# Kernel tuning notes

Hardware: AMD Instinct MI355X
Metric: run time of the kernel (lower is better)

Reference implementation:

```python
import jax, jax.numpy as jnp
import numpy as np
import math

SUB = 0.8  # fraction of input capsules kept


def _capsule_weighted_average(u):
    # u: [B, I, O, D]
    n = jnp.linalg.norm(u, axis=3, keepdims=True)          # [B, I, O, 1]
    num = jnp.sum(u * n, axis=1)                           # [B, O, D]
    den = jnp.sum(n, axis=1)                               # [B, O, 1]
    return num / den


def setup_inputs() -> dict:
    key = jax.random.key(0)
    B, I, O, D = 128, 1152, 32, 16
    u_predict = jax.random.normal(key, (B, I, O, D), dtype=jnp.float32)
    return {"u_predict": u_predict}


def reference(u_predict) -> jnp.ndarray:
    B, I, O, D = u_predict.shape
    subset_size = math.ceil(SUB * I)  # kth smallest along input_caps dim

    v = _capsule_weighted_average(u_predict)               # [B, O, D]

    # metric == 'mse': losses = -<v, u_ij> over the capsule dim
    losses = -jnp.einsum('bod,biod->bio', v, u_predict)    # [B, I, O]

    # kthvalue(k=subset_size, dim=1): k-th smallest along axis 1
    loss_threshold = jnp.sort(losses, axis=1)[:, subset_size - 1, :]  # [B, O]

    choose = (losses <= loss_threshold[:, None, :]).astype(u_predict.dtype)  # [B, I, O]
    u_masked = u_predict * choose[..., None]               # [B, I, O, D]

    return _capsule_weighted_average(u_masked)             # [B, O, D]
```

## Files before the change

kernel.cpp:

```cpp
#include <hip/hip_runtime.h>
#include <math.h>

#define BLOCK   384
#define I_CAPS  1152
#define O_CAPS  32
#define D_DIM   16
#define ROWS    3
#define K_SEL   922
#define NWAVES  6

__device__ __forceinline__ float wave_reduce_sum(float v) {
    #pragma unroll
    for (int off = 32; off > 0; off >>= 1) v += __shfl_down(v, off);
    return v;
}

__global__ __launch_bounds__(BLOCK, 3)
void subset_routing_kernel(const float* __restrict__ u, float* __restrict__ out) {
    __shared__ float red[NWAVES][17];
    __shared__ float sh_v[D_DIM];
    __shared__ int   hist[256];
    __shared__ unsigned sh_prefix;
    __shared__ int   sh_k;

    const int t    = threadIdx.x;
    const int lane = t & 63;
    const int wave = t >> 6;

    int X = blockIdx.x;
    int r = X & 7;
    int m = (X >> 3) & 1;
    int q = X >> 4;
    int p = q * 8 + r;
    int b = p >> 4;
    int o = ((p & 15) << 1) | m;

    const float4* base =
        (const float4*)u + (((size_t)b * I_CAPS) * O_CAPS + (size_t)o) * (D_DIM / 4);

    float uu[ROWS][D_DIM];
    float nn[ROWS];
    #pragma unroll
    for (int rr = 0; rr < ROWS; ++rr) {
        int i = t + rr * BLOCK;
        const float4* rowp = base + (size_t)i * (O_CAPS * (D_DIM / 4));
        float4 a0 = rowp[0], a1 = rowp[1], a2 = rowp[2], a3 = rowp[3];
        uu[rr][ 0]=a0.x; uu[rr][ 1]=a0.y; uu[rr][ 2]=a0.z; uu[rr][ 3]=a0.w;
        uu[rr][ 4]=a1.x; uu[rr][ 5]=a1.y; uu[rr][ 6]=a1.z; uu[rr][ 7]=a1.w;
        uu[rr][ 8]=a2.x; uu[rr][ 9]=a2.y; uu[rr][10]=a2.z; uu[rr][11]=a2.w;
        uu[rr][12]=a3.x; uu[rr][13]=a3.y; uu[rr][14]=a3.z; uu[rr][15]=a3.w;
    }

    float num_acc[D_DIM];
    #pragma unroll
    for (int d = 0; d < D_DIM; ++d) num_acc[d] = 0.f;
    float den_acc = 0.f;
    #pragma unroll
    for (int rr = 0; rr < ROWS; ++rr) {
        float s = 0.f;
        #pragma unroll
        for (int d = 0; d < D_DIM; ++d) s += uu[rr][d] * uu[rr][d];
        nn[rr] = sqrtf(s);
        den_acc += nn[rr];
        #pragma unroll
        for (int d = 0; d < D_DIM; ++d) num_acc[d] += uu[rr][d] * nn[rr];
    }

    #pragma unroll
    for (int d = 0; d < D_DIM; ++d) {
        float s = wave_reduce_sum(num_acc[d]);
        if (lane == 0) red[wave][d] = s;
    }
    {
        float s = wave_reduce_sum(den_acc);
        if (lane == 0) red[wave][16] = s;
    }
    __syncthreads();
    if (t < D_DIM) {
        float tot = 0.f, dtot = 0.f;
        #pragma unroll
        for (int w = 0; w < NWAVES; ++w) { tot += red[w][t]; dtot += red[w][16]; }
        sh_v[t] = tot / dtot;
    }
    __syncthreads();

    float vv[D_DIM];
    #pragma unroll
    for (int d = 0; d < D_DIM; ++d) vv[d] = sh_v[d];

    unsigned key[ROWS];
    #pragma unroll
    for (int rr = 0; rr < ROWS; ++rr) {
        float loss = 0.f;
        #pragma unroll
        for (int d = 0; d < D_DIM; ++d) loss += vv[d] * uu[rr][d];
        loss = -loss;
        unsigned bits = __float_as_uint(loss);
        unsigned msk  = ((unsigned)((int)bits >> 31)) | 0x80000000u;
        key[rr] = bits ^ msk;
    }

    unsigned prefix = 0u;
    int kk = K_SEL;
    #pragma unroll
    for (int shift = 24; shift >= 0; shift -= 8) {
        if (t < 256) hist[t] = 0;
        __syncthreads();
        unsigned maskAbove = (shift == 24) ? 0u : (0xFFFFFFFFu << (shift + 8));
        #pragma unroll
        for (int rr = 0; rr < ROWS; ++rr) {
            unsigned k = key[rr];
            if ((k & maskAbove) == prefix)
                atomicAdd(&hist[(k >> shift) & 255u], 1);
        }
        __syncthreads();
        if (wave == 0) {
            int c0 = hist[lane*4+0], c1 = hist[lane*4+1],
                c2 = hist[lane*4+2], c3 = hist[lane*4+3];
            int s = c0 + c1 + c2 + c3;
            int cum = s;
            #pragma unroll
            for (int off = 1; off < 64; off <<= 1) {
                int vsh = __shfl_up(cum, off);
                if (lane >= off) cum += vsh;
            }
            int cumprev = cum - s;
            bool has = (cumprev < kk) && (cum >= kk);
            unsigned long long ball = __ballot(has);
            int win = __ffsll(ball) - 1;
            if (lane == win) {
                int kr = kk - cumprev;
                int digit = 0;
                if (kr > c0) { kr -= c0; digit = 1;
                    if (kr > c1) { kr -= c1; digit = 2;
                        if (kr > c2) { kr -= c2; digit = 3; } } }
                sh_prefix = prefix | ((unsigned)(lane*4 + digit) << shift);
                sh_k = kr;
            }
        }
        __syncthreads();
        prefix = sh_prefix;
        kk = sh_k;
    }

    float num2[D_DIM];
    #pragma unroll
    for (int d = 0; d < D_DIM; ++d) num2[d] = 0.f;
    float den2 = 0.f;
    #pragma unroll
    for (int rr = 0; rr < ROWS; ++rr) {
        float msk = (key[rr] <= prefix) ? 1.0f : 0.0f;
        float w = nn[rr] * msk;
        den2 += w;
        #pragma unroll
        for (int d = 0; d < D_DIM; ++d) num2[d] += uu[rr][d] * w;
    }

    #pragma unroll
    for (int d = 0; d < D_DIM; ++d) {
        float s = wave_reduce_sum(num2[d]);
        if (lane == 0) red[wave][d] = s;
    }
    {
        float s = wave_reduce_sum(den2);
        if (lane == 0) red[wave][16] = s;
    }
    __syncthreads();
    if (t < D_DIM) {
        float tot = 0.f, dtot = 0.f;
        #pragma unroll
        for (int w = 0; w < NWAVES; ++w) { tot += red[w][t]; dtot += red[w][16]; }
        out[(((size_t)b * O_CAPS) + o) * D_DIM + t] = tot / dtot;
    }
}

extern "C" void kernel_launch(void* const* d_in, const int* in_sizes, int n_in,
                              void* d_out, int out_size, void* d_ws, size_t ws_size,
                              hipStream_t stream) {
    const float* u = (const float*)d_in[0];
    float* out = (float*)d_out;
    const int B = 128;
    subset_routing_kernel<<<dim3(B * O_CAPS), dim3(BLOCK), 0, stream>>>(u, out);
}
```

Baseline: 452.0 us.

## Split each capsule row across four lanes with DPP reductions

Reassigns work so four adjacent lanes each load one float4 of a 16-float capsule row, giving fully coalesced 64-byte segments per row and 12 rows per thread group. Norms and dot products are completed with DPP cross-lane swaps, and the norm is recomputed in the second pass instead of being held in registers. Because each key now appears four times, the radix-select rank and the denominator are scaled by four. The aim is better load coalescing and lower register pressure (launch bounds raised to 5) for higher occupancy, at the cost of 4x more shared-memory histogram atomics.

```diff
diff --git a/kernel.cpp b/kernel.cpp
--- a/kernel.cpp
+++ b/kernel.cpp
@@ -5,19 +5,21 @@
 #define I_CAPS  1152
 #define O_CAPS  32
 #define D_DIM   16
-#define ROWS    3
-#define K_SEL   922
+#define RPT     12
+#define K_SEL4  3688
 #define NWAVES  6
 
-__device__ __forceinline__ float wave_reduce_sum(float v) {
-    #pragma unroll
-    for (int off = 32; off > 0; off >>= 1) v += __shfl_down(v, off);
-    return v;
+__device__ __forceinline__ float dpp_xor1(float x) {
+    return __int_as_float(__builtin_amdgcn_mov_dpp(__float_as_int(x), 0xB1, 0xF, 0xF, true));
+}
+__device__ __forceinline__ float dpp_xor2(float x) {
+    return __int_as_float(__builtin_amdgcn_mov_dpp(__float_as_int(x), 0x4E, 0xF, 0xF, true));
 }
 
-__global__ __launch_bounds__(BLOCK, 3)
+__global__ __launch_bounds__(BLOCK, 5)
 void subset_routing_kernel(const float* __restrict__ u, float* __restrict__ out) {
-    __shared__ float red[NWAVES][17];
+    __shared__ float sh_num[NWAVES][16];
+    __shared__ float sh_den[NWAVES];
     __shared__ float sh_v[D_DIM];
     __shared__ int   hist[256];
     __shared__ unsigned sh_prefix;
@@ -26,90 +28,72 @@
     const int t    = threadIdx.x;
     const int lane = t & 63;
     const int wave = t >> 6;
+    const int c    = t & 3;
+    const int s    = t >> 2;
 
     int X = blockIdx.x;
-    int r = X & 7;
-    int m = (X >> 3) & 1;
-    int q = X >> 4;
-    int p = q * 8 + r;
-    int b = p >> 4;
-    int o = ((p & 15) << 1) | m;
+    int r8 = X & 7, mm = (X >> 3) & 1, q8 = X >> 4;
+    int p  = q8 * 8 + r8;
+    int b  = p >> 4;
+    int o  = ((p & 15) << 1) | mm;
 
-    const float4* base =
-        (const float4*)u + (((size_t)b * I_CAPS) * O_CAPS + (size_t)o) * (D_DIM / 4);
+    const float* base = u + (((size_t)b * I_CAPS) * O_CAPS + (size_t)o) * D_DIM + c * 4;
 
-    float uu[ROWS][D_DIM];
-    float nn[ROWS];
+    float4 q[RPT];
     #pragma unroll
-    for (int rr = 0; rr < ROWS; ++rr) {
-        int i = t + rr * BLOCK;
-        const float4* rowp = base + (size_t)i * (O_CAPS * (D_DIM / 4));
-        float4 a0 = rowp[0], a1 = rowp[1], a2 = rowp[2], a3 = rowp[3];
-        uu[rr][ 0]=a0.x; uu[rr][ 1]=a0.y; uu[rr][ 2]=a0.z; uu[rr][ 3]=a0.w;
-        uu[rr][ 4]=a1.x; uu[rr][ 5]=a1.y; uu[rr][ 6]=a1.z; uu[rr][ 7]=a1.w;
-        uu[rr][ 8]=a2.x; uu[rr][ 9]=a2.y; uu[rr][10]=a2.z; uu[rr][11]=a2.w;
-        uu[rr][12]=a3.x; uu[rr][13]=a3.y; uu[rr][14]=a3.z; uu[rr][15]=a3.w;
+    for (int r = 0; r < RPT; ++r)
+        q[r] = *(const float4*)(base + (size_t)(r * 96 + s) * (O_CAPS * D_DIM));
+
+    float ax = 0.f, ay = 0.f, az = 0.f, aw = 0.f, dn = 0.f;
+    #pragma unroll
+    for (int r = 0; r < RPT; ++r) {
+        float ss = q[r].x*q[r].x + q[r].y*q[r].y + q[r].z*q[r].z + q[r].w*q[r].w;
+        ss += dpp_xor1(ss); ss += dpp_xor2(ss);
+        float n = sqrtf(ss);
+        ax += q[r].x * n; ay += q[r].y * n; az += q[r].z * n; aw += q[r].w * n;
+        dn += n;
     }
-
-    float num_acc[D_DIM];
     #pragma unroll
-    for (int d = 0; d < D_DIM; ++d) num_acc[d] = 0.f;
-    float den_acc = 0.f;
-    #pragma unroll
-    for (int rr = 0; rr < ROWS; ++rr) {
-        float s = 0.f;
+    for (int off = 4; off < 64; off <<= 1) {
+        ax += __shfl_down(ax, off); ay += __shfl_down(ay, off);
+        az += __shfl_down(az, off); aw += __shfl_down(aw, off);
+        dn += __shfl_down(dn, off);
+    }
+    dn += dpp_xor1(dn); dn += dpp_xor2(dn);
+    if (lane < 4) {
+        float* dst = &sh_num[wave][lane * 4];
+        dst[0] = ax; dst[1] = ay; dst[2] = az; dst[3] = aw;
+    }
+    if (lane == 0) sh_den[wave] = dn;
+    __syncthreads();
+    if (t < D_DIM) {
+        float nm = 0.f, dd = 0.f;
         #pragma unroll
-        for (int d = 0; d < D_DIM; ++d) s += uu[rr][d] * uu[rr][d];
-        nn[rr] = sqrtf(s);
-        den_acc += nn[rr];
-        #pragma unroll
-        for (int d = 0; d < D_DIM; ++d) num_acc[d] += uu[rr][d] * nn[rr];
-    }
-
-    #pragma unroll
-    for (int d = 0; d < D_DIM; ++d) {
-        float s = wave_reduce_sum(num_acc[d]);
-        if (lane == 0) red[wave][d] = s;
-    }
-    {
-        float s = wave_reduce_sum(den_acc);
-        if (lane == 0) red[wave][16] = s;
+        for (int w = 0; w < NWAVES; ++w) { nm += sh_num[w][t]; dd += sh_den[w]; }
+        sh_v[t] = nm / (dd * 0.25f);
     }
     __syncthreads();
-    if (t < D_DIM) {
-        float tot = 0.f, dtot = 0.f;
-        #pragma unroll
-        for (int w = 0; w < NWAVES; ++w) { tot += red[w][t]; dtot += red[w][16]; }
-        sh_v[t] = tot / dtot;
-    }
-    __syncthreads();
+    float4 v4 = make_float4(sh_v[c*4+0], sh_v[c*4+1], sh_v[c*4+2], sh_v[c*4+3]);
 
-    float vv[D_DIM];
+    unsigned key[RPT];
     #pragma unroll
-    for (int d = 0; d < D_DIM; ++d) vv[d] = sh_v[d];
-
-    unsigned key[ROWS];
-    #pragma unroll
-    for (int rr = 0; rr < ROWS; ++rr) {
-        float loss = 0.f;
-        #pragma unroll
-        for (int d = 0; d < D_DIM; ++d) loss += vv[d] * uu[rr][d];
-        loss = -loss;
-        unsigned bits = __float_as_uint(loss);
-        unsigned msk  = ((unsigned)((int)bits >> 31)) | 0x80000000u;
-        key[rr] = bits ^ msk;
+    for (int r = 0; r < RPT; ++r) {
+        float dl = v4.x*q[r].x + v4.y*q[r].y + v4.z*q[r].z + v4.w*q[r].w;
+        dl += dpp_xor1(dl); dl += dpp_xor2(dl);
+        unsigned bits = __float_as_uint(-dl);
+        key[r] = bits ^ (((unsigned)((int)bits >> 31)) | 0x80000000u);
     }
 
     unsigned prefix = 0u;
-    int kk = K_SEL;
+    int kk = K_SEL4;
     #pragma unroll
     for (int shift = 24; shift >= 0; shift -= 8) {
         if (t < 256) hist[t] = 0;
         __syncthreads();
         unsigned maskAbove = (shift == 24) ? 0u : (0xFFFFFFFFu << (shift + 8));
         #pragma unroll
-        for (int rr = 0; rr < ROWS; ++rr) {
-            unsigned k = key[rr];
+        for (int r = 0; r < RPT; ++r) {
+            unsigned k = key[r];
             if ((k & maskAbove) == prefix)
                 atomicAdd(&hist[(k >> shift) & 255u], 1);
         }
@@ -117,14 +101,14 @@
         if (wave == 0) {
             int c0 = hist[lane*4+0], c1 = hist[lane*4+1],
                 c2 = hist[lane*4+2], c3 = hist[lane*4+3];
-            int s = c0 + c1 + c2 + c3;
-            int cum = s;
+            int sm = c0 + c1 + c2 + c3;
+            int cum = sm;
             #pragma unroll
             for (int off = 1; off < 64; off <<= 1) {
                 int vsh = __shfl_up(cum, off);
                 if (lane >= off) cum += vsh;
             }
-            int cumprev = cum - s;
+            int cumprev = cum - sm;
             bool has = (cumprev < kk) && (cum >= kk);
             unsigned long long ball = __ballot(has);
             int win = __ffsll(ball) - 1;
@@ -143,34 +127,34 @@
         kk = sh_k;
     }
 
-    float num2[D_DIM];
+    float ex = 0.f, ey = 0.f, ez = 0.f, ew = 0.f, d2 = 0.f;
     #pragma unroll
-    for (int d = 0; d < D_DIM; ++d) num2[d] = 0.f;
-    float den2 = 0.f;
+    for (int r = 0; r < RPT; ++r) {
+        float ss = q[r].x*q[r].x + q[r].y*q[r].y + q[r].z*q[r].z + q[r].w*q[r].w;
+        ss += dpp_xor1(ss); ss += dpp_xor2(ss);
+        float n = sqrtf(ss);
+        float w = (key[r] <= prefix) ? n : 0.f;
+        ex += q[r].x * w; ey += q[r].y * w; ez += q[r].z * w; ew += q[r].w * w;
+        d2 += w;
+    }
     #pragma unroll
-    for (int rr = 0; rr < ROWS; ++rr) {
-        float msk = (key[rr] <= prefix) ? 1.0f : 0.0f;
-        float w = nn[rr] * msk;
-        den2 += w;
-        #pragma unroll
-        for (int d = 0; d < D_DIM; ++d) num2[d] += uu[rr][d] * w;
+    for (int off = 4; off < 64; off <<= 1) {
+        ex += __shfl_down(ex, off); ey += __shfl_down(ey, off);
+        ez += __shfl_down(ez, off); ew += __shfl_down(ew, off);
+        d2 += __shfl_down(d2, off);
     }
-
-    #pragma unroll
-    for (int d = 0; d < D_DIM; ++d) {
-        float s = wave_reduce_sum(num2[d]);
-        if (lane == 0) red[wave][d] = s;
+    d2 += dpp_xor1(d2); d2 += dpp_xor2(d2);
+    if (lane < 4) {
+        float* dst = &sh_num[wave][lane * 4];
+        dst[0] = ex; dst[1] = ey; dst[2] = ez; dst[3] = ew;
     }
-    {
-        float s = wave_reduce_sum(den2);
-        if (lane == 0) red[wave][16] = s;
-    }
+    if (lane == 0) sh_den[wave] = d2;
     __syncthreads();
     if (t < D_DIM) {
-        float tot = 0.f, dtot = 0.f;
+        float nm = 0.f, dd = 0.f;
         #pragma unroll
-        for (int w = 0; w < NWAVES; ++w) { tot += red[w][t]; dtot += red[w][16]; }
-        out[(((size_t)b * O_CAPS) + o) * D_DIM + t] = tot / dtot;
+        for (int w = 0; w < NWAVES; ++w) { nm += sh_num[w][t]; dd += sh_den[w]; }
+        out[((size_t)b * O_CAPS + o) * D_DIM + t] = nm / (dd * 0.25f);
     }
 }
 
```

Result: no change. 444.8 us (-1.6%).
